# Kernel tuning notes

Hardware: AMD Instinct MI355X
Metric: run time of the kernel (lower is better)

## Reference

```python
import jax, jax.numpy as jnp
import numpy as np

N = 8192
DIM = 128


def setup_inputs() -> dict:
    key = jax.random.key(0)
    k1, k2 = jax.random.split(key)
    mapping = jax.random.normal(k1, (N, DIM), dtype=jnp.float32)
    # Cost matrix of the finite metric: symmetric, strictly positive off-diagonal,
    # zero diagonal (the module adds eye to the denominator to handle the diagonal).
    Draw = jax.random.uniform(k2, (N, N), dtype=jnp.float32) * 2.0 + 0.1
    D = 0.5 * (Draw + Draw.T)
    D = D * (1.0 - jnp.eye(N, dtype=jnp.float32))
    return {"mapping": mapping, "D": D}


def reference(mapping, D):
    # Pairwise Euclidean distances via GEMM formulation (||a||^2 - 2ab + ||b||^2)
    # instead of materializing the O(N^2 * dim) broadcast difference.
    n = D.shape[0]
    sq = jnp.sum(mapping * mapping, axis=-1)               # [N]
    gram = mapping @ mapping.T                             # [N, N]
    d2 = sq[:, None] + sq[None, :] - 2.0 * gram            # [N, N]
    d2 = jnp.maximum(d2, 0.0)
    # safe sqrt (exact 0 on the diagonal, matching torch.norm forward)
    pos = d2 > 0
    d = jnp.sqrt(jnp.where(pos, d2, 1.0)) * pos
    ratio = jnp.abs(d - D) / (D + jnp.eye(n, dtype=D.dtype))
    return jnp.sum(ratio) / (n * n - n)
```

## Files before the change

### kernel.cpp

```cpp
#include <hip/hip_runtime.h>
#include <math.h>

#define NN 8192
#define DIM 128
#define NG 512
#define NCT 128
#define NITEMS (NG * 16)
#define NBLOCKS 768
#define NWT (NBLOCKS * 4)

typedef short bf16x8 __attribute__((ext_vector_type(8)));
typedef float f32x4 __attribute__((ext_vector_type(4)));

__device__ inline unsigned short f2bf(float x) {
    unsigned u = __float_as_uint(x);
    unsigned r = u + 0x7FFFu + ((u >> 16) & 1u);
    return (unsigned short)(r >> 16);
}

__global__ void pack_kernel(const float* __restrict__ m, unsigned short* __restrict__ buf2) {
    const int t = threadIdx.x, l = t & 63;
    const int W = blockIdx.x * 4 + (t >> 6);
    const int g = W >> 2, kq = W & 3;
    const int row = g * 16 + (l & 15);
    const int k0 = kq * 32 + (l >> 4) * 8;
    const float* src = m + (size_t)row * DIM + k0;
    float4 v0 = *reinterpret_cast<const float4*>(src);
    float4 v1 = *reinterpret_cast<const float4*>(src + 4);
    float f[8] = {v0.x, v0.y, v0.z, v0.w, v1.x, v1.y, v1.z, v1.w};
    union { ushort4 u4[2]; unsigned short us[8]; } o;
#pragma unroll
    for (int q = 0; q < 8; ++q) o.us[q] = f2bf(f[q]);
    unsigned short* dst = buf2 + (size_t)W * 512 + l * 8;
    *reinterpret_cast<ushort4*>(dst) = o.u4[0];
    *reinterpret_cast<ushort4*>(dst + 4) = o.u4[1];
}

__global__ void sq_kernel(const float* __restrict__ mapping, float* __restrict__ sq) {
    int i = blockIdx.x * blockDim.x + threadIdx.x;
    if (i < NN) {
        const float4* row = reinterpret_cast<const float4*>(mapping + (size_t)i * DIM);
        float s = 0.f;
#pragma unroll
        for (int q = 0; q < DIM / 4; ++q) {
            float4 v = row[q];
            s += v.x * v.x + v.y * v.y + v.z * v.z + v.w * v.w;
        }
        sq[i] = s;
    }
}

__global__ __launch_bounds__(256, 3) void dist_kernel(const unsigned short* __restrict__ buf2,
                                                      const float* __restrict__ D,
                                                      const float* __restrict__ sq,
                                                      float* __restrict__ partials) {
    const int t = threadIdx.x, l = t & 63;
    const int W = blockIdx.x * 4 + (t >> 6);

    const int l15 = l & 15;
    const int colq = (l >> 4) * 4;

    int item = W;
    while (item < NITEMS) {
        const int g = item >> 4, p = item & 15;
        int cj = (g >> 2) + p;
        if (cj >= NCT) {
            if (l == 0) partials[item] = 0.f;
            item += NWT;
            continue;
        }

        const int i_row = g * 16 + l15;
        const int cdiag = g >> 2;

        bf16x8 af[4];
#pragma unroll
        for (int kq = 0; kq < 4; ++kq)
            af[kq] = *(const bf16x8*)(buf2 + (size_t)(g * 4 + kq) * 512 + l * 8);
        const float sa = sq[i_row];

        f32x4 dc[4], sbc[4];
#pragma unroll
        for (int s = 0; s < 4; ++s) {
            dc[s] = *reinterpret_cast<const f32x4*>(D + (size_t)i_row * NN + cj * 64 + s * 16 + colq);
            sbc[s] = *reinterpret_cast<const f32x4*>(sq + cj * 64 + s * 16 + colq);
        }

        float psum = 0.f;
        for (; cj < NCT; cj += 16) {
            const int ncj = cj + 16;

            bf16x8 bfr[4][4];
#pragma unroll
            for (int s = 0; s < 4; ++s)
#pragma unroll
                for (int kq = 0; kq < 4; ++kq)
                    bfr[s][kq] = *(const bf16x8*)(buf2 + (size_t)((cj * 4 + s) * 4 + kq) * 512 + l * 8);

            f32x4 dn[4], sbn[4];
            if (ncj < NCT) {
#pragma unroll
                for (int s = 0; s < 4; ++s) {
                    dn[s] = *reinterpret_cast<const f32x4*>(D + (size_t)i_row * NN + ncj * 64 + s * 16 + colq);
                    sbn[s] = *reinterpret_cast<const f32x4*>(sq + ncj * 64 + s * 16 + colq);
                }
            }

#pragma unroll
            for (int s = 0; s < 4; ++s) {
                f32x4 acc = {};
#pragma unroll
                for (int kq = 0; kq < 4; ++kq)
                    acc = __builtin_amdgcn_mfma_f32_16x16x32_bf16(bfr[s][kq], af[kq], acc, 0, 0, 0);
                if (cj != cdiag) {
#pragma unroll
                    for (int r = 0; r < 4; ++r) {
                        float d2 = fmaf(-2.f, acc[r], sa + sbc[s][r]);
                        float d = sqrtf(fmaxf(d2, 0.f));
                        float Dv = dc[s][r];
                        psum += __fdividef(fabsf(d - Dv), Dv);
                    }
                } else {
#pragma unroll
                    for (int r = 0; r < 4; ++r) {
                        const int j = cj * 64 + s * 16 + colq + r;
                        if (j > i_row) {
                            float d2 = fmaf(-2.f, acc[r], sa + sbc[s][r]);
                            float d = sqrtf(fmaxf(d2, 0.f));
                            float Dv = dc[s][r];
                            psum += __fdividef(fabsf(d - Dv), Dv);
                        }
                    }
                }
            }

            if (ncj < NCT) {
#pragma unroll
                for (int s = 0; s < 4; ++s) { dc[s] = dn[s]; sbc[s] = sbn[s]; }
            }
        }

        for (int off = 32; off > 0; off >>= 1) psum += __shfl_down(psum, off, 64);
        if (l == 0) partials[item] = 2.f * psum;

        item += NWT;
    }
}

__global__ void reduce_kernel(const float* __restrict__ partials, float* __restrict__ out) {
    __shared__ double sm[256];
    const int t = threadIdx.x;
    double s = 0.0;
    for (int i = t; i < NITEMS; i += 256) s += (double)partials[i];
    sm[t] = s;
    __syncthreads();
    for (int off = 128; off > 0; off >>= 1) {
        if (t < off) sm[t] += sm[t + off];
        __syncthreads();
    }
    if (t == 0) out[0] = (float)(sm[0] / ((double)NN * (double)NN - (double)NN));
}

extern "C" void kernel_launch(void* const* d_in, const int* in_sizes, int n_in,
                              void* d_out, int out_size, void* d_ws, size_t ws_size,
                              hipStream_t stream) {
    const float* mapping = (const float*)d_in[0];
    const float* D       = (const float*)d_in[1];
    float* out = (float*)d_out;

    unsigned short* buf2 = (unsigned short*)d_ws;
    float* sq            = (float*)(buf2 + NN * DIM);
    float* partials      = sq + NN;

    pack_kernel<<<512, 256, 0, stream>>>(mapping, buf2);
    sq_kernel<<<NN / 256, 256, 0, stream>>>(mapping, sq);
    dist_kernel<<<NBLOCKS, 256, 0, stream>>>(buf2, D, sq, partials);
    reduce_kernel<<<1, 256, 0, stream>>>(partials, out);
}
```

Baseline: 75.41 us.

## Split fused distance kernel into bf16 distance writer and D-streaming reducer

The fused MFMA-plus-D-read kernel is split in two. The first writes upper-triangle pairwise distances as bf16 into a workspace matrix. The second streams D rows with a balanced row pairing, computes the ratios and reduces per block. The aim is to separate compute-bound MFMA work from bandwidth-bound D streaming so each kernel can saturate its resource. The cost is extra global traffic: about 64MB of bf16 writes and reads (the bf16 copy covers the full matrix extent) plus further rounding of the distances to bf16.

```diff
diff --git a/kernel.cpp b/kernel.cpp
--- a/kernel.cpp
+++ b/kernel.cpp
@@ -6,8 +6,9 @@
 #define NG 512
 #define NCT 128
 #define NITEMS (NG * 16)
-#define NBLOCKS 768
-#define NWT (NBLOCKS * 4)
+#define NBLOCKS1 768
+#define NWT (NBLOCKS1 * 4)
+#define NB2 2048
 
 typedef short bf16x8 __attribute__((ext_vector_type(8)));
 typedef float f32x4 __attribute__((ext_vector_type(4)));
@@ -16,6 +17,9 @@
     unsigned u = __float_as_uint(x);
     unsigned r = u + 0x7FFFu + ((u >> 16) & 1u);
     return (unsigned short)(r >> 16);
+}
+__device__ inline float bf2f(unsigned short h) {
+    return __uint_as_float(((unsigned)h) << 16);
 }
 
 __global__ void pack_kernel(const float* __restrict__ m, unsigned short* __restrict__ buf2) {
@@ -50,28 +54,20 @@
     }
 }
 
-__global__ __launch_bounds__(256, 3) void dist_kernel(const unsigned short* __restrict__ buf2,
-                                                      const float* __restrict__ D,
-                                                      const float* __restrict__ sq,
-                                                      float* __restrict__ partials) {
+__global__ __launch_bounds__(256, 3) void dcomp_kernel(const unsigned short* __restrict__ buf2,
+                                                       const float* __restrict__ sq,
+                                                       unsigned short* __restrict__ dbuf) {
     const int t = threadIdx.x, l = t & 63;
     const int W = blockIdx.x * 4 + (t >> 6);
-
     const int l15 = l & 15;
     const int colq = (l >> 4) * 4;
 
-    int item = W;
-    while (item < NITEMS) {
+    for (int item = W; item < NITEMS; item += NWT) {
         const int g = item >> 4, p = item & 15;
         int cj = (g >> 2) + p;
-        if (cj >= NCT) {
-            if (l == 0) partials[item] = 0.f;
-            item += NWT;
-            continue;
-        }
+        if (cj >= NCT) continue;
 
         const int i_row = g * 16 + l15;
-        const int cdiag = g >> 2;
 
         bf16x8 af[4];
 #pragma unroll
@@ -79,17 +75,7 @@
             af[kq] = *(const bf16x8*)(buf2 + (size_t)(g * 4 + kq) * 512 + l * 8);
         const float sa = sq[i_row];
 
-        f32x4 dc[4], sbc[4];
-#pragma unroll
-        for (int s = 0; s < 4; ++s) {
-            dc[s] = *reinterpret_cast<const f32x4*>(D + (size_t)i_row * NN + cj * 64 + s * 16 + colq);
-            sbc[s] = *reinterpret_cast<const f32x4*>(sq + cj * 64 + s * 16 + colq);
-        }
-
-        float psum = 0.f;
         for (; cj < NCT; cj += 16) {
-            const int ncj = cj + 16;
-
             bf16x8 bfr[4][4];
 #pragma unroll
             for (int s = 0; s < 4; ++s)
@@ -97,68 +83,77 @@
                 for (int kq = 0; kq < 4; ++kq)
                     bfr[s][kq] = *(const bf16x8*)(buf2 + (size_t)((cj * 4 + s) * 4 + kq) * 512 + l * 8);
 
-            f32x4 dn[4], sbn[4];
-            if (ncj < NCT) {
-#pragma unroll
-                for (int s = 0; s < 4; ++s) {
-                    dn[s] = *reinterpret_cast<const f32x4*>(D + (size_t)i_row * NN + ncj * 64 + s * 16 + colq);
-                    sbn[s] = *reinterpret_cast<const f32x4*>(sq + ncj * 64 + s * 16 + colq);
-                }
-            }
-
 #pragma unroll
             for (int s = 0; s < 4; ++s) {
+                const int jc = cj * 64 + s * 16 + colq;
+                f32x4 sb = *reinterpret_cast<const f32x4*>(sq + jc);
                 f32x4 acc = {};
 #pragma unroll
                 for (int kq = 0; kq < 4; ++kq)
                     acc = __builtin_amdgcn_mfma_f32_16x16x32_bf16(bfr[s][kq], af[kq], acc, 0, 0, 0);
-                if (cj != cdiag) {
+                union { ushort4 u4; unsigned short us[4]; } o;
 #pragma unroll
-                    for (int r = 0; r < 4; ++r) {
-                        float d2 = fmaf(-2.f, acc[r], sa + sbc[s][r]);
-                        float d = sqrtf(fmaxf(d2, 0.f));
-                        float Dv = dc[s][r];
-                        psum += __fdividef(fabsf(d - Dv), Dv);
-                    }
-                } else {
-#pragma unroll
-                    for (int r = 0; r < 4; ++r) {
-                        const int j = cj * 64 + s * 16 + colq + r;
-                        if (j > i_row) {
-                            float d2 = fmaf(-2.f, acc[r], sa + sbc[s][r]);
-                            float d = sqrtf(fmaxf(d2, 0.f));
-                            float Dv = dc[s][r];
-                            psum += __fdividef(fabsf(d - Dv), Dv);
-                        }
-                    }
+                for (int r = 0; r < 4; ++r) {
+                    float d2 = fmaf(-2.f, acc[r], sa + sb[r]);
+                    o.us[r] = f2bf(sqrtf(fmaxf(d2, 0.f)));
                 }
-            }
-
-            if (ncj < NCT) {
-#pragma unroll
-                for (int s = 0; s < 4; ++s) { dc[s] = dn[s]; sbc[s] = sbn[s]; }
+                *reinterpret_cast<ushort4*>(dbuf + (size_t)i_row * NN + jc) = o.u4;
             }
         }
-
-        for (int off = 32; off > 0; off >>= 1) psum += __shfl_down(psum, off, 64);
-        if (l == 0) partials[item] = 2.f * psum;
-
-        item += NWT;
     }
 }
 
-__global__ void reduce_kernel(const float* __restrict__ partials, float* __restrict__ out) {
+__device__ inline void row_accum(const float* __restrict__ D,
+                                 const unsigned short* __restrict__ dbuf,
+                                 int i, int t, float& lsum) {
+    const int j0 = (i + 1) & ~3;
+    const float* Drow = D + (size_t)i * NN;
+    const unsigned short* drow = dbuf + (size_t)i * NN;
+    for (int j = j0 + t * 4; j < NN; j += 1024) {
+        float4 Dv = *reinterpret_cast<const float4*>(Drow + j);
+        ushort4 dv = *reinterpret_cast<const ushort4*>(drow + j);
+        const float Df[4] = {Dv.x, Dv.y, Dv.z, Dv.w};
+        const unsigned short du[4] = {dv.x, dv.y, dv.z, dv.w};
+#pragma unroll
+        for (int c = 0; c < 4; ++c) {
+            float r = __fdividef(fabsf(bf2f(du[c]) - Df[c]), Df[c]);
+            lsum += (j + c > i) ? r : 0.f;
+        }
+    }
+}
+
+__global__ __launch_bounds__(256, 8) void stream_kernel(const float* __restrict__ D,
+                                                        const unsigned short* __restrict__ dbuf,
+                                                        float* __restrict__ partials2) {
+    const int t = threadIdx.x, b = blockIdx.x, l = t & 63, w = t >> 6;
+    float lsum = 0.f;
+    row_accum(D, dbuf, b, t, lsum);
+    row_accum(D, dbuf, 8190 - b, t, lsum);
+    if (b < 2047) {
+        row_accum(D, dbuf, b + 2048, t, lsum);
+        row_accum(D, dbuf, 6142 - b, t, lsum);
+    }
+    if (b == 2047) row_accum(D, dbuf, 4095, t, lsum);
+
+    for (int off = 32; off > 0; off >>= 1) lsum += __shfl_down(lsum, off, 64);
+    __shared__ float wsum[4];
+    if (l == 0) wsum[w] = lsum;
+    __syncthreads();
+    if (t == 0) partials2[b] = (wsum[0] + wsum[1]) + (wsum[2] + wsum[3]);
+}
+
+__global__ void reduce_kernel(const float* __restrict__ partials2, float* __restrict__ out) {
     __shared__ double sm[256];
     const int t = threadIdx.x;
     double s = 0.0;
-    for (int i = t; i < NITEMS; i += 256) s += (double)partials[i];
+    for (int i = t; i < NB2; i += 256) s += (double)partials2[i];
     sm[t] = s;
     __syncthreads();
     for (int off = 128; off > 0; off >>= 1) {
         if (t < off) sm[t] += sm[t + off];
         __syncthreads();
     }
-    if (t == 0) out[0] = (float)(sm[0] / ((double)NN * (double)NN - (double)NN));
+    if (t == 0) out[0] = (float)(2.0 * sm[0] / ((double)NN * (double)NN - (double)NN));
 }
 
 extern "C" void kernel_launch(void* const* d_in, const int* in_sizes, int n_in,
@@ -168,12 +163,14 @@
     const float* D       = (const float*)d_in[1];
     float* out = (float*)d_out;
 
-    unsigned short* buf2 = (unsigned short*)d_ws;
-    float* sq            = (float*)(buf2 + NN * DIM);
-    float* partials      = sq + NN;
+    unsigned short* buf2    = (unsigned short*)d_ws;
+    float* sq               = (float*)(buf2 + NN * DIM);
+    float* partials2        = sq + NN;
+    unsigned short* dbuf    = (unsigned short*)(partials2 + NB2);
 
     pack_kernel<<<512, 256, 0, stream>>>(mapping, buf2);
     sq_kernel<<<NN / 256, 256, 0, stream>>>(mapping, sq);
-    dist_kernel<<<NBLOCKS, 256, 0, stream>>>(buf2, D, sq, partials);
-    reduce_kernel<<<1, 256, 0, stream>>>(partials, out);
+    dcomp_kernel<<<NBLOCKS1, 256, 0, stream>>>(buf2, sq, dbuf);
+    stream_kernel<<<NB2, 256, 0, stream>>>(D, dbuf, partials2);
+    reduce_kernel<<<1, 256, 0, stream>>>(partials2, out);
 }
```

New measurement: 99.53 us. 1.32x slower.

## Share column tiles across waves via double-buffered LDS async loads

Applied to the files above, without the earlier changes.

The persistent per-wave work loop becomes one block per 64-row strip and column-phase pair, giving 2048 blocks with a swizzled block-to-work mapping. Each wave loads a quarter of the shared B tile straight into LDS with global_load_lds, double-buffered, so all four waves reuse it instead of each reading the full tile from global memory. Manual vmcnt waits and barriers overlap the next tile's loads with the current MFMA work, and a per-block LDS reduction writes one partial. This adds barrier synchronization, relies on hand-counted wait counts, and raises occupancy to 4 blocks per SIMD.

```diff
diff --git a/kernel.cpp b/kernel.cpp
--- a/kernel.cpp
+++ b/kernel.cpp
@@ -3,14 +3,17 @@
 
 #define NN 8192
 #define DIM 128
-#define NG 512
-#define NCT 128
-#define NITEMS (NG * 16)
-#define NBLOCKS 768
-#define NWT (NBLOCKS * 4)
+#define NQ 128
+#define NP 16
+#define NBLK (NQ * NP)
 
 typedef short bf16x8 __attribute__((ext_vector_type(8)));
 typedef float f32x4 __attribute__((ext_vector_type(4)));
+
+__device__ inline void gload_lds16(const void* g, void* l) {
+    __builtin_amdgcn_global_load_lds((const __attribute__((address_space(1))) void*)g,
+                                     (__attribute__((address_space(3))) void*)l, 16, 0, 0);
+}
 
 __device__ inline unsigned short f2bf(float x) {
     unsigned u = __float_as_uint(x);
@@ -50,108 +53,125 @@
     }
 }
 
-__global__ __launch_bounds__(256, 3) void dist_kernel(const unsigned short* __restrict__ buf2,
+__global__ __launch_bounds__(256, 4) void dist_kernel(const unsigned short* __restrict__ buf2,
                                                       const float* __restrict__ D,
                                                       const float* __restrict__ sq,
                                                       float* __restrict__ partials) {
-    const int t = threadIdx.x, l = t & 63;
-    const int W = blockIdx.x * 4 + (t >> 6);
+    __shared__ __align__(16) unsigned short ldsb[2][8192];
+    __shared__ float wred[4];
 
-    const int l15 = l & 15;
-    const int colq = (l >> 4) * 4;
+    const int t = threadIdx.x, l = t & 63, w = t >> 6;
+    const int b = blockIdx.x;
+    const int nb = (b & 7) * (NBLK / 8) + (b >> 3);
+    const int q = nb >> 4, p = nb & 15;
+    const int cj0 = q + p;
 
-    int item = W;
-    while (item < NITEMS) {
-        const int g = item >> 4, p = item & 15;
-        int cj = (g >> 2) + p;
-        if (cj >= NCT) {
-            if (l == 0) partials[item] = 0.f;
-            item += NWT;
-            continue;
-        }
+    float psum = 0.f;
 
-        const int i_row = g * 16 + l15;
-        const int cdiag = g >> 2;
+    if (cj0 < 128) {
+        const int nt = (128 - cj0 + 15) >> 4;
+        const int l15 = l & 15, colq = (l >> 4) * 4;
+        const int i_row = q * 64 + w * 16 + l15;
 
         bf16x8 af[4];
 #pragma unroll
         for (int kq = 0; kq < 4; ++kq)
-            af[kq] = *(const bf16x8*)(buf2 + (size_t)(g * 4 + kq) * 512 + l * 8);
+            af[kq] = *(const bf16x8*)(buf2 + (size_t)(((q * 4 + w) * 4) + kq) * 512 + l * 8);
         const float sa = sq[i_row];
 
-        f32x4 dc[4], sbc[4];
+        f32x4 dcA[4], dcB[4];
 #pragma unroll
-        for (int s = 0; s < 4; ++s) {
-            dc[s] = *reinterpret_cast<const f32x4*>(D + (size_t)i_row * NN + cj * 64 + s * 16 + colq);
-            sbc[s] = *reinterpret_cast<const f32x4*>(sq + cj * 64 + s * 16 + colq);
-        }
+        for (int kq = 0; kq < 4; ++kq)
+            gload_lds16(buf2 + (size_t)((cj0 * 4 + w) * 4 + kq) * 512 + l * 8,
+                        (void*)&ldsb[0][(w * 4 + kq) * 512]);
+#pragma unroll
+        for (int s = 0; s < 4; ++s)
+            dcA[s] = *(const f32x4*)(D + (size_t)i_row * NN + cj0 * 64 + s * 16 + colq);
 
-        float psum = 0.f;
-        for (; cj < NCT; cj += 16) {
-            const int ncj = cj + 16;
+        auto step = [&](int tt, f32x4(&dc)[4], f32x4(&dn)[4], int cur) {
+            const int cj = cj0 + tt * 16;
+            const bool more = (tt + 1 < nt);
 
-            bf16x8 bfr[4][4];
+            f32x4 sbc[4];
 #pragma unroll
             for (int s = 0; s < 4; ++s)
+                sbc[s] = *(const f32x4*)(sq + cj * 64 + s * 16 + colq);
+            if (more) {
+                const int ncj = cj + 16;
 #pragma unroll
                 for (int kq = 0; kq < 4; ++kq)
-                    bfr[s][kq] = *(const bf16x8*)(buf2 + (size_t)((cj * 4 + s) * 4 + kq) * 512 + l * 8);
+                    gload_lds16(buf2 + (size_t)((ncj * 4 + w) * 4 + kq) * 512 + l * 8,
+                                (void*)&ldsb[cur ^ 1][(w * 4 + kq) * 512]);
+#pragma unroll
+                for (int s = 0; s < 4; ++s)
+                    dn[s] = *(const f32x4*)(D + (size_t)i_row * NN + ncj * 64 + s * 16 + colq);
+            }
+            __builtin_amdgcn_sched_barrier(0);
+            if (more) asm volatile("s_waitcnt vmcnt(16)" ::: "memory");
+            else      asm volatile("s_waitcnt vmcnt(8)" ::: "memory");
+            __builtin_amdgcn_s_barrier();
 
-            f32x4 dn[4], sbn[4];
-            if (ncj < NCT) {
-#pragma unroll
-                for (int s = 0; s < 4; ++s) {
-                    dn[s] = *reinterpret_cast<const f32x4*>(D + (size_t)i_row * NN + ncj * 64 + s * 16 + colq);
-                    sbn[s] = *reinterpret_cast<const f32x4*>(sq + ncj * 64 + s * 16 + colq);
-                }
-            }
-
+            f32x4 acc[4];
 #pragma unroll
             for (int s = 0; s < 4; ++s) {
-                f32x4 acc = {};
+                bf16x8 bfr[4];
 #pragma unroll
                 for (int kq = 0; kq < 4; ++kq)
-                    acc = __builtin_amdgcn_mfma_f32_16x16x32_bf16(bfr[s][kq], af[kq], acc, 0, 0, 0);
-                if (cj != cdiag) {
+                    bfr[kq] = *(const bf16x8*)&ldsb[cur][(s * 4 + kq) * 512 + l * 8];
+                f32x4 a = {};
+#pragma unroll
+                for (int kq = 0; kq < 4; ++kq)
+                    a = __builtin_amdgcn_mfma_f32_16x16x32_bf16(bfr[kq], af[kq], a, 0, 0, 0);
+                acc[s] = a;
+            }
+            asm volatile("s_waitcnt lgkmcnt(0)" ::: "memory");
+            __builtin_amdgcn_sched_barrier(0);
+            __builtin_amdgcn_s_barrier();
+
+            if (cj != q) {
+#pragma unroll
+                for (int s = 0; s < 4; ++s)
 #pragma unroll
                     for (int r = 0; r < 4; ++r) {
-                        float d2 = fmaf(-2.f, acc[r], sa + sbc[s][r]);
+                        float d2 = fmaf(-2.f, acc[s][r], sa + sbc[s][r]);
                         float d = sqrtf(fmaxf(d2, 0.f));
                         float Dv = dc[s][r];
                         psum += __fdividef(fabsf(d - Dv), Dv);
                     }
-                } else {
+            } else {
+#pragma unroll
+                for (int s = 0; s < 4; ++s)
 #pragma unroll
                     for (int r = 0; r < 4; ++r) {
                         const int j = cj * 64 + s * 16 + colq + r;
                         if (j > i_row) {
-                            float d2 = fmaf(-2.f, acc[r], sa + sbc[s][r]);
+                            float d2 = fmaf(-2.f, acc[s][r], sa + sbc[s][r]);
                             float d = sqrtf(fmaxf(d2, 0.f));
                             float Dv = dc[s][r];
                             psum += __fdividef(fabsf(d - Dv), Dv);
                         }
                     }
-                }
             }
+        };
 
-            if (ncj < NCT) {
-#pragma unroll
-                for (int s = 0; s < 4; ++s) { dc[s] = dn[s]; sbc[s] = sbn[s]; }
-            }
+        for (int tt = 0; tt < nt; tt += 2) {
+            step(tt, dcA, dcB, 0);
+            if (tt + 1 < nt) step(tt + 1, dcB, dcA, 1);
         }
+    }
 
-        for (int off = 32; off > 0; off >>= 1) psum += __shfl_down(psum, off, 64);
-        if (l == 0) partials[item] = 2.f * psum;
-
-        item += NWT;
-    }
+    for (int off = 32; off > 0; off >>= 1) psum += __shfl_down(psum, off, 64);
+    __syncthreads();
+    if (l == 0) wred[w] = psum;
+    __syncthreads();
+    if (t == 0) partials[b] = 2.f * ((wred[0] + wred[1]) + (wred[2] + wred[3]));
 }
 
 __global__ void reduce_kernel(const float* __restrict__ partials, float* __restrict__ out) {
     __shared__ double sm[256];
     const int t = threadIdx.x;
     double s = 0.0;
-    for (int i = t; i < NITEMS; i += 256) s += (double)partials[i];
+    for (int i = t; i < NBLK; i += 256) s += (double)partials[i];
     sm[t] = s;
     __syncthreads();
     for (int off = 128; off > 0; off >>= 1) {
@@ -174,6 +194,6 @@
 
     pack_kernel<<<512, 256, 0, stream>>>(mapping, buf2);
     sq_kernel<<<NN / 256, 256, 0, stream>>>(mapping, sq);
-    dist_kernel<<<NBLOCKS, 256, 0, stream>>>(buf2, D, sq, partials);
+    dist_kernel<<<NBLK, 256, 0, stream>>>(buf2, D, sq, partials);
     reduce_kernel<<<1, 256, 0, stream>>>(partials, out);
 }
```

After: 91.02 us. 1.21x slower.
